# Performance work log

Hardware: AMD Instinct MI355X
Metric: run time of the kernel (lower is better)

Reference implementation:

```python
import jax, jax.numpy as jnp
import numpy as np

B, S, D, H = 8, 1024, 1024, 16
DH = D // H
LN_EPS = 1e-5


def setup_inputs() -> dict:
    key = jax.random.key(0)
    ks = jax.random.split(key, 12)
    lim = 1.0 / np.sqrt(D)
    u = lambda k, shp: jax.random.uniform(k, shp, jnp.float32, -lim, lim)
    return {
        "x": jax.random.normal(ks[0], (B, S, D), jnp.float32),
        "Wq": u(ks[1], (D, D)), "bq": u(ks[2], (D,)),
        "Wk": u(ks[3], (D, D)), "bk": u(ks[4], (D,)),
        "Wv": u(ks[5], (D, D)), "bv": u(ks[6], (D,)),
        "Wo": u(ks[7], (D, D)), "bo": u(ks[8], (D,)),
        "gamma": jnp.ones((D,), jnp.float32),
        "beta": jnp.zeros((D,), jnp.float32),
        "num_head": H,
    }


def reference(x, Wq, bq, Wk, bk, Wv, bv, Wo, bo, gamma, beta, num_head):
    b, s, d = x.shape
    dh = d // num_head
    # projections (torch Linear: y = x @ W.T + b)
    Q = x @ Wq.T + bq
    K = x @ Wk.T + bk
    V = x @ Wv.T + bv
    # faithful raw row-major reshape [B, S, D] -> [B*H, S, DH] (as in the
    # original .view, which does NOT do a proper head split/transpose)
    Q = Q.reshape(b * num_head, -1, dh)
    K = K.reshape(b * num_head, -1, dh)
    V = V.reshape(b * num_head, -1, dh)
    scale = dh ** (-0.5)
    scores = jnp.einsum('bqd,bkd->bqk', Q, K) * scale  # [B*H, S, S]
    alpha = jax.nn.softmax(scores, axis=-1)
    context = jnp.einsum('bqk,bkd->bqd', alpha, V)
    context = context.reshape(b, -1, dh * num_head)
    out = context @ Wo.T + bo
    # dropout is identity in eval mode
    out = out + x
    mu = jnp.mean(out, axis=-1, keepdims=True)
    var = jnp.var(out, axis=-1, keepdims=True)
    out = (out - mu) * jax.lax.rsqrt(var + LN_EPS) * gamma + beta
    return out, alpha
```

## Files before the change

kernel.cpp:

```cpp
#include <hip/hip_runtime.h>
#include <stdint.h>
#include <math.h>

typedef __bf16 bf16_t;
typedef float f32x4 __attribute__((ext_vector_type(4)));
typedef float f32x2 __attribute__((ext_vector_type(2)));
typedef __bf16 bf16x8 __attribute__((ext_vector_type(8)));
typedef __bf16 bf16x4 __attribute__((ext_vector_type(4)));

#define D_ 1024
#define M_ 8192

__device__ __forceinline__ f32x4 mfma16(bf16x8 a, bf16x8 b, f32x4 c) {
  return __builtin_amdgcn_mfma_f32_16x16x32_bf16(a, b, c, 0, 0, 0);
}

__device__ __forceinline__ void gl_lds16(const bf16_t* g, bf16_t* l) {
  __builtin_amdgcn_global_load_lds(
      (const __attribute__((address_space(1))) unsigned int*)g,
      (__attribute__((address_space(3))) unsigned int*)l, 16, 0, 0);
}

__global__ __launch_bounds__(256) void cvt_all(
    const float* __restrict__ x,
    const float* __restrict__ w0, const float* __restrict__ w1,
    const float* __restrict__ w2, const float* __restrict__ w3,
    bf16_t* __restrict__ xb,
    bf16_t* __restrict__ d0, bf16_t* __restrict__ d1,
    bf16_t* __restrict__ d2, bf16_t* __restrict__ d3) {
  int b = blockIdx.x;
  const float* s;
  bf16_t* d;
  int i;
  if (b < 4096) {
    s = x; d = xb; i = b * 256 + threadIdx.x;
  } else {
    int g = b - 4096;
    int which = g >> 9;
    s = which == 0 ? w0 : which == 1 ? w1 : which == 2 ? w2 : w3;
    d = which == 0 ? d0 : which == 1 ? d1 : which == 2 ? d2 : d3;
    i = (g & 511) * 256 + threadIdx.x;
  }
  const f32x4* p = (const f32x4*)(s + (size_t)i * 8);
  f32x4 a = p[0], bb = p[1];
  bf16x8 o;
  o[0] = (bf16_t)a.x; o[1] = (bf16_t)a.y; o[2] = (bf16_t)a.z; o[3] = (bf16_t)a.w;
  o[4] = (bf16_t)bb.x; o[5] = (bf16_t)bb.y; o[6] = (bf16_t)bb.z; o[7] = (bf16_t)bb.w;
  *(bf16x8*)(d + (size_t)i * 8) = o;
}

__device__ __forceinline__ void gemm_core(const bf16_t* __restrict__ A,
                                          const bf16_t* __restrict__ W,
                                          int m0, int n0,
                                          bf16_t* As, bf16_t* Bs,
                                          f32x4 acc[4][4]) {
  const int t = threadIdx.x;
  const int l = t & 63, w = t >> 6;
  const int wr = w >> 1, wc = w & 1;
  const int lr = l & 15, lg = l >> 4;
  const int srow = t >> 2;
  const int scol = (t & 3) * 8;
  const bf16_t* gA0 = A + (size_t)(m0 + srow) * D_ + scol;
  const bf16_t* gA1 = A + (size_t)(m0 + 64 + srow) * D_ + scol;
  const bf16_t* gB0 = W + (size_t)(n0 + srow) * D_ + scol;
  const bf16_t* gB1 = W + (size_t)(n0 + 64 + srow) * D_ + scol;

  for (int k0 = 0; k0 < D_; k0 += 32) {
    gl_lds16(gA0 + k0, As + t * 8);
    gl_lds16(gA1 + k0, As + 2048 + t * 8);
    gl_lds16(gB0 + k0, Bs + t * 8);
    gl_lds16(gB1 + k0, Bs + 2048 + t * 8);
    __syncthreads();
    bf16x8 af[4], bfr[4];
#pragma unroll
    for (int i = 0; i < 4; ++i)
      af[i] = *(const bf16x8*)(As + (wr * 64 + i * 16 + lr) * 32 + lg * 8);
#pragma unroll
    for (int i = 0; i < 4; ++i)
      bfr[i] = *(const bf16x8*)(Bs + (wc * 64 + i * 16 + lr) * 32 + lg * 8);
#pragma unroll
    for (int mi = 0; mi < 4; ++mi)
#pragma unroll
      for (int ni = 0; ni < 4; ++ni)
        acc[mi][ni] = mfma16(af[mi], bfr[ni], acc[mi][ni]);
    __syncthreads();
  }
}

__global__ __launch_bounds__(256) void gemm_qkv(
    const bf16_t* __restrict__ A,
    const bf16_t* __restrict__ Wq, const bf16_t* __restrict__ Wk, const bf16_t* __restrict__ Wv,
    const float* __restrict__ bq, const float* __restrict__ bk, const float* __restrict__ bv,
    bf16_t* __restrict__ Oq, bf16_t* __restrict__ Ok, bf16_t* __restrict__ Ov) {
  __shared__ bf16_t As[128 * 32], Bs[128 * 32];
  int z = blockIdx.z;
  const bf16_t* W = z == 0 ? Wq : (z == 1 ? Wk : Wv);
  const float* bias = z == 0 ? bq : (z == 1 ? bk : bv);
  bf16_t* O = z == 0 ? Oq : (z == 1 ? Ok : Ov);
  float scale = z == 0 ? 0.18033688f : 1.0f;
  int m0 = blockIdx.y * 128, n0 = blockIdx.x * 128;
  f32x4 acc[4][4] = {};
  gemm_core(A, W, m0, n0, As, Bs, acc);
  int t = threadIdx.x, l = t & 63, w = t >> 6;
  int wr = w >> 1, wc = w & 1, lr = l & 15, lg = l >> 4;
#pragma unroll
  for (int mi = 0; mi < 4; ++mi) {
#pragma unroll
    for (int ni = 0; ni < 4; ++ni) {
      int col = n0 + wc * 64 + ni * 16 + lr;
      float bb = bias[col];
      int row = m0 + wr * 64 + mi * 16 + lg * 4;
      bf16_t* op = O + (size_t)row * D_ + col;
#pragma unroll
      for (int r = 0; r < 4; ++r)
        op[(size_t)r * D_] = (bf16_t)((acc[mi][ni][r] + bb) * scale);
    }
  }
}

__global__ __launch_bounds__(256) void gemm_proj(
    const bf16_t* __restrict__ A, const bf16_t* __restrict__ W,
    const float* __restrict__ bias, const float* __restrict__ xres,
    float* __restrict__ O) {
  __shared__ bf16_t As[128 * 32], Bs[128 * 32];
  int m0 = blockIdx.y * 128, n0 = blockIdx.x * 128;
  f32x4 acc[4][4] = {};
  gemm_core(A, W, m0, n0, As, Bs, acc);
  int t = threadIdx.x, l = t & 63, w = t >> 6;
  int wr = w >> 1, wc = w & 1, lr = l & 15, lg = l >> 4;
#pragma unroll
  for (int mi = 0; mi < 4; ++mi) {
#pragma unroll
    for (int ni = 0; ni < 4; ++ni) {
      int col = n0 + wc * 64 + ni * 16 + lr;
      float bb = bias[col];
      int row = m0 + wr * 64 + mi * 16 + lg * 4;
#pragma unroll
      for (int r = 0; r < 4; ++r) {
        size_t idx = (size_t)(row + r) * D_ + col;
        O[idx] = acc[mi][ni][r] + bb + xres[idx];
      }
    }
  }
}

__global__ __launch_bounds__(256) void transpose_v(const bf16_t* __restrict__ V,
                                                   bf16_t* __restrict__ Vt) {
  __shared__ float sT[128 * 33];
  int bh = blockIdx.x >> 3, st = blockIdx.x & 7;
  int s0 = st * 128;
  int t = threadIdx.x;
  const bf16_t* src = V + (size_t)bh * 65536 + (size_t)s0 * 64;
  int li = t >> 3, lc = t & 7;
#pragma unroll
  for (int p = 0; p < 4; ++p) {
    int row = p * 32 + li;
    f32x4 v = *(const f32x4*)(src + (size_t)row * 64 + lc * 8);
    float* dst = &sT[row * 33 + lc * 4];
    dst[0] = v[0]; dst[1] = v[1]; dst[2] = v[2]; dst[3] = v[3];
  }
  __syncthreads();
  int sc = t & 15, dh0 = t >> 4;
  bf16_t* dstb = Vt + (size_t)bh * 65536;
#pragma unroll
  for (int p = 0; p < 4; ++p) {
    int dh = dh0 + p * 16;
    bf16x8 o;
#pragma unroll
    for (int j = 0; j < 8; ++j) {
      int s = sc * 8 + j;
      o[j] = ((const bf16_t*)&sT[s * 33 + (dh >> 1)])[dh & 1];
    }
    *(bf16x8*)(dstb + (size_t)dh * 1024 + s0 + sc * 8) = o;
  }
}

#define SP_STRIDE 1064
__global__ __launch_bounds__(512, 4) void attn_kernel(
    const bf16_t* __restrict__ Q, const bf16_t* __restrict__ K,
    const bf16_t* __restrict__ Vt, float* __restrict__ alpha,
    bf16_t* __restrict__ ctx) {
  __shared__ bf16_t sP[32][SP_STRIDE];
  __shared__ float sRS[8][32];
  __shared__ float sL[32];

  int id = blockIdx.x;
  int g = id >> 3, x = id & 7;
  int qt = g & 31;
  int bh = ((g >> 5) << 3) | x;
  int q0 = qt * 32;

  const bf16_t* Qb = Q + (size_t)bh * 65536;
  const bf16_t* Kb = K + (size_t)bh * 65536;
  const bf16_t* Vb = Vt + (size_t)bh * 65536;
  float* Ab = alpha + (size_t)bh * 1048576 + (size_t)q0 * 1024;

  int t = threadIdx.x, l = t & 63, w = t >> 6;
  int lr = l & 15, lg = l >> 4;

  bf16x8 qa[2][2];
#pragma unroll
  for (int mi = 0; mi < 2; ++mi)
#pragma unroll
    for (int kk = 0; kk < 2; ++kk)
      qa[mi][kk] = *(const bf16x8*)(Qb + (size_t)(q0 + mi * 16 + lr) * 64 + kk * 32 + lg * 8);

  float pa0 = 0.f, pa1 = 0.f;
#pragma unroll
  for (int tt = 0; tt < 8; ++tt) {
    int n0 = w * 128 + tt * 16;
    bf16x8 kb0 = *(const bf16x8*)(Kb + (size_t)(n0 + lr) * 64 + lg * 8);
    bf16x8 kb1 = *(const bf16x8*)(Kb + (size_t)(n0 + lr) * 64 + 32 + lg * 8);
    f32x4 a0 = {0.f, 0.f, 0.f, 0.f};
    f32x4 a1 = {0.f, 0.f, 0.f, 0.f};
    a0 = mfma16(kb0, qa[0][0], a0);
    a0 = mfma16(kb1, qa[0][1], a0);
    a1 = mfma16(kb0, qa[1][0], a1);
    a1 = mfma16(kb1, qa[1][1], a1);
    bf16x4 w0, w1;
#pragma unroll
    for (int r = 0; r < 4; ++r) {
      float e0 = exp2f(a0[r]);
      float e1 = exp2f(a1[r]);
      pa0 += e0; pa1 += e1;
      w0[r] = (bf16_t)e0;
      w1[r] = (bf16_t)e1;
    }
    *(bf16x4*)&sP[lr][n0 + lg * 4] = w0;
    *(bf16x4*)&sP[16 + lr][n0 + lg * 4] = w1;
  }
  pa0 += __shfl_xor(pa0, 16); pa0 += __shfl_xor(pa0, 32);
  pa1 += __shfl_xor(pa1, 16); pa1 += __shfl_xor(pa1, 32);
  if (l < 16) {
    sRS[w][lr] = pa0;
    sRS[w][16 + lr] = pa1;
  }
  __syncthreads();
  if (t < 32) {
    float s = 0.f;
#pragma unroll
    for (int ww = 0; ww < 8; ++ww) s += sRS[ww][t];
    sL[t] = 1.0f / s;
  }
  __syncthreads();

  {
    int wm = w >> 2, wn = w & 3;
    f32x4 acc = {0.f, 0.f, 0.f, 0.f};
    const bf16_t* vp = Vb + (size_t)(wn * 16 + lr) * 1024 + lg * 8;
    const bf16_t* pp = &sP[wm * 16 + lr][lg * 8];
    int arow = t >> 4, acol = (t & 15) * 4;
    float inv = sL[arow];
    const bf16_t* ap = &sP[arow][acol];
    float* aout = Ab + (size_t)arow * 1024 + acol;
#pragma unroll 4
    for (int n0 = 0; n0 < 1024; n0 += 64) {
      bf16x8 ea0 = *(const bf16x8*)(pp + n0);
      bf16x8 vb0 = *(const bf16x8*)(vp + n0);
      acc = mfma16(ea0, vb0, acc);
      bf16x8 ea1 = *(const bf16x8*)(pp + n0 + 32);
      bf16x8 vb1 = *(const bf16x8*)(vp + n0 + 32);
      acc = mfma16(ea1, vb1, acc);
      bf16x4 p = *(const bf16x4*)(ap + n0);
      f32x4 o;
      o[0] = (float)p[0] * inv;
      o[1] = (float)p[1] * inv;
      o[2] = (float)p[2] * inv;
      o[3] = (float)p[3] * inv;
      __builtin_nontemporal_store(o, (f32x4*)(aout + n0));
    }
    bf16_t* cp = ctx + (size_t)bh * 65536 + (size_t)(q0 + wm * 16 + lg * 4) * 64 + wn * 16 + lr;
#pragma unroll
    for (int r = 0; r < 4; ++r)
      cp[(size_t)r * 64] = (bf16_t)(acc[r] * sL[wm * 16 + lg * 4 + r]);
  }
}

__global__ __launch_bounds__(256) void ln_kernel(float* __restrict__ io,
                                                 const float* __restrict__ gamma,
                                                 const float* __restrict__ beta) {
  int row = blockIdx.x;
  int t = threadIdx.x;
  float* p = io + (size_t)row * 1024;
  f32x4 v = *(const f32x4*)(p + t * 4);
  float s = v[0] + v[1] + v[2] + v[3];
  float s2 = v[0] * v[0] + v[1] * v[1] + v[2] * v[2] + v[3] * v[3];
#pragma unroll
  for (int off = 1; off <= 32; off <<= 1) {
    s += __shfl_xor(s, off);
    s2 += __shfl_xor(s2, off);
  }
  __shared__ float ps[4], ps2[4];
  int w = t >> 6, l = t & 63;
  if (l == 0) { ps[w] = s; ps2[w] = s2; }
  __syncthreads();
  float S = ps[0] + ps[1] + ps[2] + ps[3];
  float S2 = ps2[0] + ps2[1] + ps2[2] + ps2[3];
  float mu = S * (1.f / 1024.f);
  float var = S2 * (1.f / 1024.f) - mu * mu;
  float rs = rsqrtf(var + 1e-5f);
  f32x4 g = *(const f32x4*)(gamma + t * 4);
  f32x4 b = *(const f32x4*)(beta + t * 4);
  f32x4 o;
  o[0] = (v[0] - mu) * rs * g[0] + b[0];
  o[1] = (v[1] - mu) * rs * g[1] + b[1];
  o[2] = (v[2] - mu) * rs * g[2] + b[2];
  o[3] = (v[3] - mu) * rs * g[3] + b[3];
  *(f32x4*)(p + t * 4) = o;
}

extern "C" void kernel_launch(void* const* d_in, const int* in_sizes, int n_in,
                              void* d_out, int out_size, void* d_ws, size_t ws_size,
                              hipStream_t stream) {
  const float* x = (const float*)d_in[0];
  const float* Wq = (const float*)d_in[1];
  const float* bq = (const float*)d_in[2];
  const float* Wk = (const float*)d_in[3];
  const float* bk = (const float*)d_in[4];
  const float* Wv = (const float*)d_in[5];
  const float* bv = (const float*)d_in[6];
  const float* Wo = (const float*)d_in[7];
  const float* bo = (const float*)d_in[8];
  const float* gamma = (const float*)d_in[9];
  const float* beta = (const float*)d_in[10];

  char* ws = (char*)d_ws;
  size_t off = 0;
  bf16_t* xb = (bf16_t*)(ws + off);  off += (size_t)M_ * D_ * 2;
  bf16_t* Wqb = (bf16_t*)(ws + off); off += (size_t)D_ * D_ * 2;
  bf16_t* Wkb = (bf16_t*)(ws + off); off += (size_t)D_ * D_ * 2;
  bf16_t* Wvb = (bf16_t*)(ws + off); off += (size_t)D_ * D_ * 2;
  bf16_t* Wob = (bf16_t*)(ws + off); off += (size_t)D_ * D_ * 2;
  bf16_t* Qb = (bf16_t*)(ws + off);  off += (size_t)M_ * D_ * 2;
  bf16_t* Kb = (bf16_t*)(ws + off);  off += (size_t)M_ * D_ * 2;
  bf16_t* Vb = (bf16_t*)(ws + off);  off += (size_t)M_ * D_ * 2;
  bf16_t* Vtb = (bf16_t*)(ws + off); off += (size_t)M_ * D_ * 2;
  bf16_t* ctxb = (bf16_t*)(ws + off); off += (size_t)M_ * D_ * 2;

  float* out0 = (float*)d_out;
  float* alpha = out0 + (size_t)M_ * D_;

  cvt_all<<<6144, 256, 0, stream>>>(x, Wq, Wk, Wv, Wo, xb, Wqb, Wkb, Wvb, Wob);

  gemm_qkv<<<dim3(8, 64, 3), 256, 0, stream>>>(xb, Wqb, Wkb, Wvb, bq, bk, bv, Qb, Kb, Vb);
  transpose_v<<<1024, 256, 0, stream>>>(Vb, Vtb);
  attn_kernel<<<4096, 512, 0, stream>>>(Qb, Kb, Vtb, alpha, ctxb);
  gemm_proj<<<dim3(8, 64), 256, 0, stream>>>(ctxb, Wob, bo, x, out0);
  ln_kernel<<<8192, 256, 0, stream>>>(out0, gamma, beta);
}
```

Measured before the change: 333.4 us.

## Replace QKV GEMM with 256x256-tile, 8-wave, double-buffered pipelined kernel

The fused QKV projection now uses 256x256 output tiles computed by 512-thread workgroups, with a 128 KB double-buffered LDS pipeline fed by global_load_lds. Staging of the next K-slices is interleaved with MFMA quads, ordered by explicit vmcnt waits and barriers, and the MFMA sections run at raised wave priority. LDS addresses are XOR-swizzled to avoid bank conflicts, and the workgroup index is remapped so that blocks sharing a tile are spread across XCDs. The aim is higher MFMA utilisation and more operand reuse than the old 128x128 single-buffered loop. In exchange, the hand-tuned wait counts are fragile and the large LDS footprint limits occupancy to one block per CU.

```diff
diff --git a/kernel.cpp b/kernel.cpp
--- a/kernel.cpp
+++ b/kernel.cpp
@@ -4,7 +4,6 @@
 
 typedef __bf16 bf16_t;
 typedef float f32x4 __attribute__((ext_vector_type(4)));
-typedef float f32x2 __attribute__((ext_vector_type(2)));
 typedef __bf16 bf16x8 __attribute__((ext_vector_type(8)));
 typedef __bf16 bf16x4 __attribute__((ext_vector_type(4)));
 
@@ -49,6 +48,135 @@
   *(bf16x8*)(d + (size_t)i * 8) = o;
 }
 
+#define LDSB(e) (*(const bf16x8*)(Sm + (e)))
+
+#define STG_AH(b, h, kt)                                                      \
+  {                                                                           \
+    gl_lds16(A + sA + (h) * 131072 + (kt) * 64,                               \
+             Sm + (b) * 32768 + (h) * 8192 + tid * 8);                        \
+    gl_lds16(A + sA + (h) * 131072 + 65536 + (kt) * 64,                       \
+             Sm + (b) * 32768 + (h) * 8192 + 4096 + tid * 8);                 \
+  }
+#define STG_BH(b, h, kt)                                                      \
+  {                                                                           \
+    gl_lds16(Wsel + sB + (h) * 131072 + (kt) * 64,                            \
+             Sm + (b) * 32768 + 16384 + (h) * 8192 + tid * 8);                \
+    gl_lds16(Wsel + sB + (h) * 131072 + 65536 + (kt) * 64,                    \
+             Sm + (b) * 32768 + 16384 + (h) * 8192 + 4096 + tid * 8);         \
+  }
+
+#define QUAD(B, S0, S1, S2, S3)                                               \
+  {                                                                           \
+    const int bb = (B) * 32768;                                               \
+    _Pragma("unroll") for (int q = 0; q < 4; ++q) {                           \
+      if (q == 0) {                                                           \
+        _Pragma("unroll") for (int fn = 0; fn < 4; ++fn) {                    \
+          bfr[fn][0] = LDSB(bb + bBase + fn * 1024);                          \
+          bfr[fn][1] = LDSB(bb + bBase + fn * 1024 + 32);                     \
+        }                                                                     \
+      }                                                                       \
+      bf16x8 af[2][2];                                                        \
+      _Pragma("unroll") for (int mi = 0; mi < 2; ++mi) {                      \
+        af[mi][0] = LDSB(bb + aBase + (2 * q + mi) * 1024);                   \
+        af[mi][1] = LDSB(bb + aBase + (2 * q + mi) * 1024 + 32);              \
+      }                                                                       \
+      if (q == 0) { S0; } else if (q == 1) { S1; }                            \
+      else if (q == 2) { S2; } else { S3; }                                   \
+      __builtin_amdgcn_s_barrier();                                           \
+      __builtin_amdgcn_s_setprio(1);                                          \
+      _Pragma("unroll") for (int mi = 0; mi < 2; ++mi)                        \
+      _Pragma("unroll") for (int fn = 0; fn < 4; ++fn) {                      \
+        acc[2 * q + mi][fn] =                                                 \
+            mfma16(af[mi][0], bfr[fn][0], acc[2 * q + mi][fn]);               \
+        acc[2 * q + mi][fn] =                                                 \
+            mfma16(af[mi][1], bfr[fn][1], acc[2 * q + mi][fn]);               \
+      }                                                                       \
+      __builtin_amdgcn_s_setprio(0);                                          \
+      __builtin_amdgcn_s_barrier();                                           \
+    }                                                                         \
+  }
+
+__global__ __launch_bounds__(512) void gemm_qkv8(
+    const bf16_t* __restrict__ A,
+    const bf16_t* __restrict__ Wq, const bf16_t* __restrict__ Wk,
+    const bf16_t* __restrict__ Wv,
+    const float* __restrict__ bq, const float* __restrict__ bk,
+    const float* __restrict__ bv,
+    bf16_t* __restrict__ Oq, bf16_t* __restrict__ Ok, bf16_t* __restrict__ Ov) {
+  __shared__ bf16_t Sm[65536];
+
+  const int tid = threadIdx.x;
+  const int l = tid & 63, w = tid >> 6;
+  const int wm = w >> 2, wn = w & 3;
+  const int lr = l & 15, lg = l >> 4;
+
+  int wg = blockIdx.x;
+  int nid = (wg & 7) * 48 + (wg >> 3);
+  int bm = nid & 31, bnid = nid >> 5;
+  int which = bnid >> 2;
+  const bf16_t* Wsel = which == 0 ? Wq : (which == 1 ? Wk : Wv);
+  const float* bias = which == 0 ? bq : (which == 1 ? bk : bv);
+  bf16_t* O = which == 0 ? Oq : (which == 1 ? Ok : Ov);
+  const float scale = which == 0 ? 0.18033688f : 1.0f;
+  const int m0 = bm * 256, n0 = (bnid & 3) * 256;
+
+  const int scol = ((l & 7) ^ (((l >> 5) & 1) << 1)) * 8;
+  const int sA = (m0 + w * 8 + (l >> 3)) * 1024 + scol;
+  const int sB = (n0 + w * 8 + (l >> 3)) * 1024 + scol;
+
+  const int eCol = (lg * 8) ^ ((lr & 4) << 2);
+  const int aBase = wm * 8192 + lr * 64 + eCol;
+  const int bBase = 16384 + (wn >> 1) * 8192 + ((wn & 1) * 64 + lr) * 64 + eCol;
+
+  f32x4 acc[8][4] = {};
+  bf16x8 bfr[4][2];
+
+  STG_AH(0, 0, 0) STG_AH(0, 1, 0) STG_BH(0, 0, 0) STG_BH(0, 1, 0)
+  STG_BH(1, 0, 1) STG_BH(1, 1, 1) STG_AH(1, 0, 1)
+  asm volatile("s_waitcnt vmcnt(6)" ::: "memory");
+  __builtin_amdgcn_sched_barrier(0);
+  __builtin_amdgcn_s_barrier();
+
+  for (int i = 0; i < 8; ++i) {
+    const bool st = (i < 7);
+    const int k2 = 2 * i + 2, k3 = 2 * i + 3;
+    QUAD(0,
+         STG_AH(1, 1, 2 * i + 1),
+         if (st) STG_BH(0, 0, k2),
+         if (st) STG_BH(0, 1, k2),
+         if (st) STG_AH(0, 0, k2))
+    if (i < 7) {
+      asm volatile("s_waitcnt vmcnt(6)" ::: "memory");
+    } else {
+      asm volatile("s_waitcnt vmcnt(0)" ::: "memory");
+    }
+    __builtin_amdgcn_sched_barrier(0);
+    QUAD(1,
+         if (st) STG_AH(0, 1, k2),
+         if (st) STG_BH(1, 0, k3),
+         if (st) STG_BH(1, 1, k3),
+         if (st) STG_AH(1, 0, k3))
+    if (i < 7) {
+      asm volatile("s_waitcnt vmcnt(6)" ::: "memory");
+      __builtin_amdgcn_sched_barrier(0);
+    }
+  }
+
+#pragma unroll
+  for (int fn = 0; fn < 4; ++fn) {
+    int col = n0 + wn * 64 + fn * 16 + lr;
+    float bb2 = bias[col];
+#pragma unroll
+    for (int fm = 0; fm < 8; ++fm) {
+      int row = m0 + wm * 128 + fm * 16 + lg * 4;
+      bf16_t* op = O + (size_t)row * 1024 + col;
+#pragma unroll
+      for (int r = 0; r < 4; ++r)
+        op[(size_t)r * 1024] = (bf16_t)((acc[fm][fn][r] + bb2) * scale);
+    }
+  }
+}
+
 __device__ __forceinline__ void gemm_core(const bf16_t* __restrict__ A,
                                           const bf16_t* __restrict__ W,
                                           int m0, int n0,
@@ -84,37 +212,6 @@
       for (int ni = 0; ni < 4; ++ni)
         acc[mi][ni] = mfma16(af[mi], bfr[ni], acc[mi][ni]);
     __syncthreads();
-  }
-}
-
-__global__ __launch_bounds__(256) void gemm_qkv(
-    const bf16_t* __restrict__ A,
-    const bf16_t* __restrict__ Wq, const bf16_t* __restrict__ Wk, const bf16_t* __restrict__ Wv,
-    const float* __restrict__ bq, const float* __restrict__ bk, const float* __restrict__ bv,
-    bf16_t* __restrict__ Oq, bf16_t* __restrict__ Ok, bf16_t* __restrict__ Ov) {
-  __shared__ bf16_t As[128 * 32], Bs[128 * 32];
-  int z = blockIdx.z;
-  const bf16_t* W = z == 0 ? Wq : (z == 1 ? Wk : Wv);
-  const float* bias = z == 0 ? bq : (z == 1 ? bk : bv);
-  bf16_t* O = z == 0 ? Oq : (z == 1 ? Ok : Ov);
-  float scale = z == 0 ? 0.18033688f : 1.0f;
-  int m0 = blockIdx.y * 128, n0 = blockIdx.x * 128;
-  f32x4 acc[4][4] = {};
-  gemm_core(A, W, m0, n0, As, Bs, acc);
-  int t = threadIdx.x, l = t & 63, w = t >> 6;
-  int wr = w >> 1, wc = w & 1, lr = l & 15, lg = l >> 4;
-#pragma unroll
-  for (int mi = 0; mi < 4; ++mi) {
-#pragma unroll
-    for (int ni = 0; ni < 4; ++ni) {
-      int col = n0 + wc * 64 + ni * 16 + lr;
-      float bb = bias[col];
-      int row = m0 + wr * 64 + mi * 16 + lg * 4;
-      bf16_t* op = O + (size_t)row * D_ + col;
-#pragma unroll
-      for (int r = 0; r < 4; ++r)
-        op[(size_t)r * D_] = (bf16_t)((acc[mi][ni][r] + bb) * scale);
-    }
   }
 }
 
@@ -342,7 +439,7 @@
 
   cvt_all<<<6144, 256, 0, stream>>>(x, Wq, Wk, Wv, Wo, xb, Wqb, Wkb, Wvb, Wob);
 
-  gemm_qkv<<<dim3(8, 64, 3), 256, 0, stream>>>(xb, Wqb, Wkb, Wvb, bq, bk, bv, Qb, Kb, Vb);
+  gemm_qkv8<<<384, 512, 0, stream>>>(xb, Wqb, Wkb, Wvb, bq, bk, bv, Qb, Kb, Vb);
   transpose_v<<<1024, 256, 0, stream>>>(Vb, Vtb);
   attn_kernel<<<4096, 512, 0, stream>>>(Qb, Kb, Vtb, alpha, ctxb);
   gemm_proj<<<dim3(8, 64), 256, 0, stream>>>(ctxb, Wob, bo, x, out0);
```

New measurement: 335.1 us. No clear change (+0.5%).

## Rewrite QKV projection GEMM with 256x256 tiles, double-buffered LDS and XCD-aware mapping

Applied to the files above, without the earlier changes.

Replaces the 128x128, K=32 QKV GEMM with a 512-thread kernel using 256x256 output tiles and K=64 steps. Tiles are double-buffered in 128KB of LDS so the next tile loads while the current one computes, with XOR-swizzled LDS addressing to avoid bank conflicts. Blocks are remapped so neighbouring M tiles share an XCD for L2 reuse. Larger tiles raise arithmetic intensity and halve the barrier count per K, but launch only 384 blocks at one block per CU, which cuts occupancy and may leave some CUs idle.

```diff
diff --git a/kernel.cpp b/kernel.cpp
--- a/kernel.cpp
+++ b/kernel.cpp
@@ -4,7 +4,6 @@
 
 typedef __bf16 bf16_t;
 typedef float f32x4 __attribute__((ext_vector_type(4)));
-typedef float f32x2 __attribute__((ext_vector_type(2)));
 typedef __bf16 bf16x8 __attribute__((ext_vector_type(8)));
 typedef __bf16 bf16x4 __attribute__((ext_vector_type(4)));
 
@@ -49,6 +48,97 @@
   *(bf16x8*)(d + (size_t)i * 8) = o;
 }
 
+#define LDSB(e) (*(const bf16x8*)(Sm + (e)))
+
+#define STG2(b, kt)                                                          \
+  {                                                                          \
+    _Pragma("unroll") for (int c = 0; c < 4; ++c) {                          \
+      gl_lds16(A + (size_t)(m0 + c * 64 + srow) * 1024 + (kt) * 64 + scol,   \
+               Sm + (b) * 32768 + c * 4096 + tid * 8);                       \
+      gl_lds16(Wsel + (size_t)(n0 + c * 64 + srow) * 1024 + (kt) * 64 + scol,\
+               Sm + (b) * 32768 + 16384 + c * 4096 + tid * 8);               \
+    }                                                                        \
+  }
+
+__global__ __launch_bounds__(512) void gemm_qkv2(
+    const bf16_t* __restrict__ A,
+    const bf16_t* __restrict__ Wq, const bf16_t* __restrict__ Wk,
+    const bf16_t* __restrict__ Wv,
+    const float* __restrict__ bq, const float* __restrict__ bk,
+    const float* __restrict__ bv,
+    bf16_t* __restrict__ Oq, bf16_t* __restrict__ Ok, bf16_t* __restrict__ Ov) {
+  __shared__ bf16_t Sm[65536];
+
+  const int tid = threadIdx.x;
+  const int l = tid & 63, w = tid >> 6;
+  const int wm = w >> 2, wn = w & 3;
+  const int lr = l & 15, lg = l >> 4;
+
+  int wg = blockIdx.x;
+  int xcd = wg & 7, local = wg >> 3;
+  int bm = xcd * 4 + (local & 3);
+  int bnid = local >> 2;
+  int which = bnid >> 2;
+  const bf16_t* Wsel = which == 0 ? Wq : (which == 1 ? Wk : Wv);
+  const float* bias = which == 0 ? bq : (which == 1 ? bk : bv);
+  bf16_t* O = which == 0 ? Oq : (which == 1 ? Ok : Ov);
+  const float scale = which == 0 ? 0.18033688f : 1.0f;
+  const int m0 = bm * 256, n0 = (bnid & 3) * 256;
+
+  const int scol = ((l & 7) ^ ((l >> 3) & 7)) * 8;
+  const int srow = w * 8 + (l >> 3);
+
+  const int rdA = (wm * 128 + lr) * 64 + (lg ^ (lr & 7)) * 8;
+  const int rdB = 16384 + (wn * 64 + lr) * 64 + (lg ^ (lr & 7)) * 8;
+
+  f32x4 acc[8][4] = {};
+
+  STG2(0, 0)
+  asm volatile("s_waitcnt vmcnt(0)" ::: "memory");
+  __builtin_amdgcn_sched_barrier(0);
+  __builtin_amdgcn_s_barrier();
+
+  int cur = 0;
+  for (int kt = 0; kt < 16; ++kt) {
+    if (kt < 15) STG2(cur ^ 1, kt + 1)
+    const int bb = cur * 32768;
+    bf16x8 bfr[4][2];
+#pragma unroll
+    for (int fn = 0; fn < 4; ++fn) {
+      bfr[fn][0] = LDSB(bb + rdB + fn * 1024);
+      bfr[fn][1] = LDSB((bb + rdB + fn * 1024) ^ 32);
+    }
+#pragma unroll
+    for (int fm = 0; fm < 8; ++fm) {
+      bf16x8 a0 = LDSB(bb + rdA + fm * 1024);
+      bf16x8 a1 = LDSB((bb + rdA + fm * 1024) ^ 32);
+#pragma unroll
+      for (int fn = 0; fn < 4; ++fn) {
+        acc[fm][fn] = mfma16(a0, bfr[fn][0], acc[fm][fn]);
+        acc[fm][fn] = mfma16(a1, bfr[fn][1], acc[fm][fn]);
+      }
+    }
+    asm volatile("s_waitcnt vmcnt(0)" ::: "memory");
+    __builtin_amdgcn_sched_barrier(0);
+    __builtin_amdgcn_s_barrier();
+    cur ^= 1;
+  }
+
+#pragma unroll
+  for (int fn = 0; fn < 4; ++fn) {
+    int col = n0 + wn * 64 + fn * 16 + lr;
+    float bb2 = bias[col];
+#pragma unroll
+    for (int fm = 0; fm < 8; ++fm) {
+      int row = m0 + wm * 128 + fm * 16 + lg * 4;
+      bf16_t* op = O + (size_t)row * 1024 + col;
+#pragma unroll
+      for (int r = 0; r < 4; ++r)
+        op[(size_t)r * 1024] = (bf16_t)((acc[fm][fn][r] + bb2) * scale);
+    }
+  }
+}
+
 __device__ __forceinline__ void gemm_core(const bf16_t* __restrict__ A,
                                           const bf16_t* __restrict__ W,
                                           int m0, int n0,
@@ -84,37 +174,6 @@
       for (int ni = 0; ni < 4; ++ni)
         acc[mi][ni] = mfma16(af[mi], bfr[ni], acc[mi][ni]);
     __syncthreads();
-  }
-}
-
-__global__ __launch_bounds__(256) void gemm_qkv(
-    const bf16_t* __restrict__ A,
-    const bf16_t* __restrict__ Wq, const bf16_t* __restrict__ Wk, const bf16_t* __restrict__ Wv,
-    const float* __restrict__ bq, const float* __restrict__ bk, const float* __restrict__ bv,
-    bf16_t* __restrict__ Oq, bf16_t* __restrict__ Ok, bf16_t* __restrict__ Ov) {
-  __shared__ bf16_t As[128 * 32], Bs[128 * 32];
-  int z = blockIdx.z;
-  const bf16_t* W = z == 0 ? Wq : (z == 1 ? Wk : Wv);
-  const float* bias = z == 0 ? bq : (z == 1 ? bk : bv);
-  bf16_t* O = z == 0 ? Oq : (z == 1 ? Ok : Ov);
-  float scale = z == 0 ? 0.18033688f : 1.0f;
-  int m0 = blockIdx.y * 128, n0 = blockIdx.x * 128;
-  f32x4 acc[4][4] = {};
-  gemm_core(A, W, m0, n0, As, Bs, acc);
-  int t = threadIdx.x, l = t & 63, w = t >> 6;
-  int wr = w >> 1, wc = w & 1, lr = l & 15, lg = l >> 4;
-#pragma unroll
-  for (int mi = 0; mi < 4; ++mi) {
-#pragma unroll
-    for (int ni = 0; ni < 4; ++ni) {
-      int col = n0 + wc * 64 + ni * 16 + lr;
-      float bb = bias[col];
-      int row = m0 + wr * 64 + mi * 16 + lg * 4;
-      bf16_t* op = O + (size_t)row * D_ + col;
-#pragma unroll
-      for (int r = 0; r < 4; ++r)
-        op[(size_t)r * D_] = (bf16_t)((acc[mi][ni][r] + bb) * scale);
-    }
   }
 }
 
@@ -342,7 +401,7 @@
 
   cvt_all<<<6144, 256, 0, stream>>>(x, Wq, Wk, Wv, Wo, xb, Wqb, Wkb, Wvb, Wob);
 
-  gemm_qkv<<<dim3(8, 64, 3), 256, 0, stream>>>(xb, Wqb, Wkb, Wvb, bq, bk, bv, Qb, Kb, Vb);
+  gemm_qkv2<<<384, 512, 0, stream>>>(xb, Wqb, Wkb, Wvb, bq, bk, bv, Qb, Kb, Vb);
   transpose_v<<<1024, 256, 0, stream>>>(Vb, Vtb);
   attn_kernel<<<4096, 512, 0, stream>>>(Qb, Kb, Vtb, alpha, ctxb);
   gemm_proj<<<dim3(8, 64), 256, 0, stream>>>(ctxb, Wob, bo, x, out0);
```

Result: no change. 331.0 us (-0.7%).
